# Kernel optimization log

Measured on AMD Instinct MI355X. Metric: run time of the kernel, lower is better.

## Reference

```python
import jax, jax.numpy as jnp
import numpy as np

CHEB_K = 3
DIM_IN = 2
HIDDEN = 64
EMBED_DIM = 10
NODE_NUM = 2048
BATCH = 32


def _gconv(x, supports, W, b, cheb_k=CHEB_K):
    # Chebyshev graph conv applied directly to x (equivalent to building
    # T_k(A) matrices then applying: T_k(A) x = 2 A T_{k-1}(A) x - T_{k-2}(A) x).
    xs = [x, jnp.einsum('nm,bmc->bnc', supports, x)]
    for _ in range(2, cheb_k):
        xs.append(2.0 * jnp.einsum('nm,bmc->bnc', supports, xs[-1]) - xs[-2])
    x_g = jnp.concatenate(xs, axis=-1)          # [B, N, cheb_k*C]
    return jnp.einsum('bni,io->bno', x_g, W) + b


def setup_inputs() -> dict:
    key = jax.random.key(0)
    ks = jax.random.split(key, 7)
    c_in = DIM_IN + HIDDEN                       # 66
    # xavier_normal-ish scale for weights
    def xavier(k, fan_in, fan_out):
        std = float(np.sqrt(2.0 / (fan_in + fan_out)))
        return jax.random.normal(k, (fan_in, fan_out), dtype=jnp.float32) * std
    return {
        'x': jax.random.normal(ks[0], (BATCH, NODE_NUM, DIM_IN), dtype=jnp.float32),
        'state': jax.random.normal(ks[1], (BATCH, NODE_NUM, HIDDEN), dtype=jnp.float32),
        'node_embeddings': jax.random.normal(ks[2], (NODE_NUM, EMBED_DIM), dtype=jnp.float32),
        'W_gate': xavier(ks[3], CHEB_K * c_in, 2 * HIDDEN),
        'b_gate': jnp.zeros((2 * HIDDEN,), dtype=jnp.float32),
        'W_update': xavier(ks[4], CHEB_K * c_in, HIDDEN),
        'b_update': jnp.zeros((HIDDEN,), dtype=jnp.float32),
    }


def reference(x, state, node_embeddings, W_gate, b_gate, W_update, b_update):
    # adaptive adjacency: softmax(relu(E E^T), axis=1)
    logits = jnp.einsum('nc,mc->nm', node_embeddings, node_embeddings)
    supports = jax.nn.softmax(jax.nn.relu(logits), axis=1)   # [N, N]

    input_and_state = jnp.concatenate([x, state], axis=-1)   # [B, N, dim_in+hidden]
    z_r = jax.nn.sigmoid(_gconv(input_and_state, supports, W_gate, b_gate))
    z, r = jnp.split(z_r, 2, axis=-1)                        # each [B, N, hidden]
    candidate = jnp.concatenate([x, z * state], axis=-1)
    hc = jnp.tanh(_gconv(candidate, supports, W_update, b_update))
    h = r * state + (1.0 - r) * hc
    return h
```

## Files before the change

### kernel.cpp

```cpp
#include <hip/hip_runtime.h>


typedef __bf16 bf16x8 __attribute__((ext_vector_type(8)));
typedef __bf16 bf16x4 __attribute__((ext_vector_type(4)));
typedef __bf16 bf16x2 __attribute__((ext_vector_type(2)));
typedef float  f32x4  __attribute__((ext_vector_type(4)));

#define GLB(p) ((__attribute__((address_space(1))) void*)(void*)(p))
#define LDS(p) ((__attribute__((address_space(3))) void*)(p))

__global__ __launch_bounds__(256, 2)
void prologue_kernel(const float* __restrict__ E, __bf16* __restrict__ S,
                     const float* __restrict__ Wg, __bf16* __restrict__ WTg,
                     const float* __restrict__ Wu, __bf16* __restrict__ WTu,
                     const float* __restrict__ x, const float* __restrict__ st,
                     __bf16* __restrict__ T, __bf16* __restrict__ G) {
    const int bid = blockIdx.x;
    const int t = threadIdx.x;
    __shared__ float Ls[66 * 129];
    if (bid >= 2304) {
        const int rb = bid - 2304;
        const int b  = rb >> 4;
        const int n0 = (rb & 15) << 7;
        const size_t mb = (size_t)b * 2048 + n0;
        if (t < 128) {
            const float2 v = *(const float2*)&x[(mb + t) * 2];
            Ls[t] = v.x;
            Ls[129 + t] = v.y;
        }
#pragma unroll
        for (int r = 0; r < 8; ++r) {
            const int task = r * 256 + t;
            const int q = task & 15, n = task >> 4;
            f32x4 v = *(const f32x4*)&st[(mb + n) * 64 + q * 4];
            const int base = (2 + q * 4) * 129 + n;
#pragma unroll
            for (int j = 0; j < 4; ++j) Ls[base + j * 129] = v[j];
        }
        __syncthreads();
#pragma unroll
        for (int r = 0; r < 5; ++r) {
            const int task = r * 256 + t;
            if (task < 1056) {
                const int c = task >> 4, seg = task & 15;
                const float* src = &Ls[c * 129 + seg * 8];
                bf16x8 o;
#pragma unroll
                for (int j = 0; j < 8; ++j) o[j] = (__bf16)src[j];
                *(bf16x8*)&T[(size_t)(b * 66 + c) * 2048 + n0 + seg * 8] = o;
            }
        }
        {
            const int n = t & 127, half = t >> 7;
            const size_t grow = ((size_t)(b * 2048 + n0 + n)) * 256;
            for (int oct = half * 5; oct < (half ? 9 : 5); ++oct) {
                bf16x8 o8;
#pragma unroll
                for (int j = 0; j < 8; ++j) {
                    const int cc = oct * 8 + j;
                    o8[j] = (cc < 66) ? (__bf16)Ls[cc * 129 + n] : (__bf16)0.f;
                }
                *(bf16x8*)&G[grow + oct * 8] = o8;
            }
        }
        return;
    }
    if (bid >= 2048) {
        const float* W = (bid < 2176) ? Wg : Wu;
        __bf16* WT = (bid < 2176) ? WTg : WTu;
        const int Nout = (bid < 2176) ? 128 : 64;
        const int id = (bid - ((bid < 2176) ? 2048 : 2176)) * 256 + t;
        const int o = id >> 8, k = id & 255;
        const int jj = (k >= 144) ? 2 : (k >= 72 ? 1 : 0);
        const int cc = k - 72 * jj;
        const bool ok = (o < Nout) && (cc < 66) && (k < 216);
        float v = 0.f;
        if (ok) {
            if (jj == 0)      v = W[(size_t)cc * Nout + o] - W[(size_t)(132 + cc) * Nout + o];
            else if (jj == 1) v = W[(size_t)(66 + cc) * Nout + o];
            else              v = 2.f * W[(size_t)(132 + cc) * Nout + o];
        }
        WT[id] = (__bf16)v;
        return;
    }
    const int n = bid;
    const int l = t & 63, w = t >> 6;
    float* sm = Ls;
    float* ss = Ls + 4;
    float en[10];
#pragma unroll
    for (int i = 0; i < 10; ++i) en[i] = E[n * 10 + i];
    float vals[8];
    float mx = 0.f;
#pragma unroll
    for (int q = 0; q < 8; ++q) {
        const int m = q * 256 + t;
        const float* em = E + (size_t)m * 10;
        float d = 0.f;
#pragma unroll
        for (int i = 0; i < 10; ++i) d += en[i] * em[i];
        d = fmaxf(d, 0.f);
        vals[q] = d;
        mx = fmaxf(mx, d);
    }
#pragma unroll
    for (int off = 32; off; off >>= 1) mx = fmaxf(mx, __shfl_xor(mx, off));
    if (l == 0) sm[w] = mx;
    __syncthreads();
    mx = fmaxf(fmaxf(sm[0], sm[1]), fmaxf(sm[2], sm[3]));
    float sum = 0.f;
#pragma unroll
    for (int q = 0; q < 8; ++q) { vals[q] = __expf(vals[q] - mx); sum += vals[q]; }
#pragma unroll
    for (int off = 32; off; off >>= 1) sum += __shfl_xor(sum, off);
    if (l == 0) ss[w] = sum;
    __syncthreads();
    sum = ss[0] + ss[1] + ss[2] + ss[3];
    const float inv = 1.f / sum;
#pragma unroll
    for (int q = 0; q < 8; ++q) S[(size_t)n * 2048 + q * 256 + t] = (__bf16)(vals[q] * inv);
}

__global__ __launch_bounds__(256, 3)
void gemm_pipe(const __bf16* __restrict__ A, int lda,
               const __bf16* __restrict__ Bt, int ldb,
               int K, int epi, int swz, int cmode,
               __bf16* __restrict__ outT,
               float* __restrict__ outF, const float* __restrict__ bias,
               const __bf16* __restrict__ zrI,
               const float* __restrict__ state,
               __bf16* __restrict__ Gout, int gsec) {
    __shared__ __align__(16) __bf16 As[2][128 * 64];
    __shared__ __align__(16) __bf16 Bs[2][64 * 64];
    int mt, ct;
    if (swz) { mt = blockIdx.x & 15; ct = blockIdx.x >> 4; }
    else     { mt = blockIdx.x;      ct = blockIdx.y; }
    const int m0 = mt * 128, c0 = ct * 64;
    const int t = threadIdx.x;
    const int l = t & 63, w = t >> 6;
    const int wr = w >> 1, wc = w & 1;
    const int lm = l & 15, kq = l >> 4, lm7 = lm & 7;
    const int sr = l >> 3;
    const int gsw = (l & 7) ^ sr;

    f32x4 acc[4][2];
#pragma unroll
    for (int i = 0; i < 4; ++i)
#pragma unroll
        for (int j = 0; j < 2; ++j) acc[i][j] = (f32x4)0.f;

    const __bf16* Asrc = A  + (size_t)(m0 + w * 8 + sr) * lda + gsw * 8;
    const __bf16* Bsrc = Bt + (size_t)(c0 + w * 8 + sr) * ldb + gsw * 8;
    const int dstA = w * 512 + l * 8;

    auto stage = [&](int buf, int k0) {
#pragma unroll
        for (int q = 0; q < 4; ++q)
            __builtin_amdgcn_global_load_lds(GLB(Asrc + (size_t)q * 32 * lda + k0),
                                             LDS(&As[buf][q * 2048 + dstA]), 16, 0, 0);
#pragma unroll
        for (int q = 0; q < 2; ++q)
            __builtin_amdgcn_global_load_lds(GLB(Bsrc + (size_t)q * 32 * ldb + k0),
                                             LDS(&Bs[buf][q * 2048 + dstA]), 16, 0, 0);
    };
    auto compute = [&](int buf) {
        const __bf16* Ab = &As[buf][0];
        const __bf16* Bb = &Bs[buf][0];
#pragma unroll
        for (int ks = 0; ks < 2; ++ks) {
            const int ga = (((ks << 2) | kq) ^ lm7) << 3;
            bf16x8 af[4], bfr[2];
#pragma unroll
            for (int i = 0; i < 4; ++i)
                af[i] = *(const bf16x8*)&Ab[(wr * 64 + i * 16 + lm) * 64 + ga];
#pragma unroll
            for (int j = 0; j < 2; ++j)
                bfr[j] = *(const bf16x8*)&Bb[(wc * 32 + j * 16 + lm) * 64 + ga];
#pragma unroll
            for (int i = 0; i < 4; ++i)
#pragma unroll
                for (int j = 0; j < 2; ++j)
                    acc[i][j] = __builtin_amdgcn_mfma_f32_16x16x32_bf16(af[i], bfr[j], acc[i][j], 0, 0, 0);
        }
    };

    stage(0, 0);
    const int iters = K >> 6;
    for (int i = 0; i + 2 <= iters; i += 2) {
        stage(1, (i + 1) << 6);
        __builtin_amdgcn_sched_barrier(0);
        __builtin_amdgcn_s_waitcnt(0x0F76);
        __builtin_amdgcn_s_barrier();
        __builtin_amdgcn_sched_barrier(0);
        compute(0);
        __builtin_amdgcn_sched_barrier(0);
        __builtin_amdgcn_s_barrier();
        __builtin_amdgcn_sched_barrier(0);
        if (i + 2 < iters) {
            stage(0, (i + 2) << 6);
            __builtin_amdgcn_sched_barrier(0);
            __builtin_amdgcn_s_waitcnt(0x0F76);
        } else {
            __builtin_amdgcn_s_waitcnt(0x0F70);
        }
        __builtin_amdgcn_s_barrier();
        __builtin_amdgcn_sched_barrier(0);
        compute(1);
        __builtin_amdgcn_sched_barrier(0);
        if (i + 4 <= iters) {
            __builtin_amdgcn_s_barrier();
            __builtin_amdgcn_sched_barrier(0);
        }
    }

    const int rb0 = m0 + wr * 64 + kq * 4;
    const int cb0 = c0 + wc * 32 + lm;
    __bf16* Lt = &As[0][0];
#pragma unroll
    for (int i = 0; i < 4; ++i) {
        const int rbase = rb0 + i * 16;
#pragma unroll
        for (int j = 0; j < 2; ++j) {
            const int c = cb0 + j * 16;
            f32x4 v = acc[i][j];
            if (epi <= 1) {
                bf16x4 pk;
#pragma unroll
                for (int r = 0; r < 4; ++r) pk[r] = (__bf16)v[r];
                if (epi == 0)
                    *(bf16x4*)&outT[(size_t)c * 2048 + rbase] = pk;
                const int mbL = wr * 64 + kq * 4 + i * 16;
                const int clocb = wc * 32 + lm + j * 16;
#pragma unroll
                for (int r = 0; r < 4; ++r) {
                    const int ml = mbL + r;
                    const int swr = (ml & 7) ^ ((ml >> 3) & 7);
                    Lt[ml * 64 + ((((clocb >> 3) ^ swr) & 7) << 3) + (clocb & 7)] = pk[r];
                }
            } else {
                if (c < 64) {
                    const float bb = bias[c];
#pragma unroll
                    for (int r = 0; r < 4; ++r) {
                        const int m = rbase + r;
                        float xx = fminf(fmaxf(v[r] + bb, -15.f), 15.f);
                        float e = __expf(2.f * xx);
                        float hc = (e - 1.f) / (e + 1.f);
                        float rr = (float)zrI[(size_t)m * 64 + c];
                        float s = state[(size_t)m * 64 + c];
                        outF[(size_t)m * 64 + c] = rr * s + (1.f - rr) * hc;
                    }
                }
            }
        }
    }
    if (epi <= 1) {
        __syncthreads();
        const int mloc = t >> 1, h = t & 1;
        const int m = m0 + mloc;
        const int sw = (mloc & 7) ^ ((mloc >> 3) & 7);
#pragma unroll
        for (int k = 0; k < 4; ++k) {
            const int g = h * 4 + k;
            const bf16x8 v = *(const bf16x8*)&Lt[mloc * 64 + ((g ^ sw) & 7) * 8];
            const int c = c0 + g * 8;
            if (cmode) {
                const int b = c >> 6;
                *(bf16x8*)&Gout[((size_t)(b * 2048 + m)) * 256 + gsec + 2 + (c & 63)] = v;
            } else {
                const int b0 = c / 66, b7 = (c + 7) / 66;
                if (b0 == b7) {
                    *(bf16x8*)&Gout[((size_t)(b0 * 2048 + m)) * 256 + gsec + (c - b0 * 66)] = v;
                } else {
#pragma unroll
                    for (int e = 0; e < 8; ++e) {
                        const int ce = c + e, be = ce / 66;
                        Gout[((size_t)(be * 2048 + m)) * 256 + gsec + (ce - be * 66)] = v[e];
                    }
                }
            }
        }
    }
}

__global__ __launch_bounds__(256, 2)
void gemm_w(const __bf16* __restrict__ A,
            const __bf16* __restrict__ Bt,
            __bf16* __restrict__ outT, const float* __restrict__ bias,
            __bf16* __restrict__ zrO,
            const float* __restrict__ state,
            __bf16* __restrict__ Gout,
            const float* __restrict__ xin) {
    __shared__ __align__(16) __bf16 As[2][128 * 64];
    __shared__ __align__(16) __bf16 Bs[2][128 * 64];
    const int m0 = blockIdx.x * 128;
    const int t = threadIdx.x;
    const int l = t & 63, w = t >> 6;
    const int wr = w >> 1, wc = w & 1;
    const int lm = l & 15, kq = l >> 4, lm7 = lm & 7;
    const int sr = l >> 3;
    const int gsw = (l & 7) ^ sr;

    f32x4 acc[4][4];
#pragma unroll
    for (int i = 0; i < 4; ++i)
#pragma unroll
        for (int j = 0; j < 4; ++j) acc[i][j] = (f32x4)0.f;

    const __bf16* Asrc = A  + (size_t)(m0 + w * 8 + sr) * 256 + gsw * 8;
    const __bf16* Bsrc = Bt + (size_t)(w * 8 + sr) * 256 + gsw * 8;
    const int dstA = w * 512 + l * 8;

    auto stage = [&](int buf, int k0) {
#pragma unroll
        for (int q = 0; q < 4; ++q)
            __builtin_amdgcn_global_load_lds(GLB(Asrc + (size_t)q * 32 * 256 + k0),
                                             LDS(&As[buf][q * 2048 + dstA]), 16, 0, 0);
#pragma unroll
        for (int q = 0; q < 4; ++q)
            __builtin_amdgcn_global_load_lds(GLB(Bsrc + (size_t)q * 32 * 256 + k0),
                                             LDS(&Bs[buf][q * 2048 + dstA]), 16, 0, 0);
    };
    auto compute = [&](int buf) {
        const __bf16* Ab = &As[buf][0];
        const __bf16* Bb = &Bs[buf][0];
#pragma unroll
        for (int ks = 0; ks < 2; ++ks) {
            const int ga = (((ks << 2) | kq) ^ lm7) << 3;
            bf16x8 af[4], bfr[4];
#pragma unroll
            for (int i = 0; i < 4; ++i)
                af[i] = *(const bf16x8*)&Ab[(wr * 64 + i * 16 + lm) * 64 + ga];
#pragma unroll
            for (int j = 0; j < 4; ++j)
                bfr[j] = *(const bf16x8*)&Bb[(wc * 64 + j * 16 + lm) * 64 + ga];
#pragma unroll
            for (int i = 0; i < 4; ++i)
#pragma unroll
                for (int j = 0; j < 4; ++j)
                    acc[i][j] = __builtin_amdgcn_mfma_f32_16x16x32_bf16(af[i], bfr[j], acc[i][j], 0, 0, 0);
        }
    };

    stage(0, 0);
    const int iters = 4;
    for (int i = 0; i + 2 <= iters; i += 2) {
        stage(1, (i + 1) << 6);
        __builtin_amdgcn_sched_barrier(0);
        __builtin_amdgcn_s_waitcnt(0x0F78);
        __builtin_amdgcn_s_barrier();
        __builtin_amdgcn_sched_barrier(0);
        compute(0);
        __builtin_amdgcn_sched_barrier(0);
        __builtin_amdgcn_s_barrier();
        __builtin_amdgcn_sched_barrier(0);
        if (i + 2 < iters) {
            stage(0, (i + 2) << 6);
            __builtin_amdgcn_sched_barrier(0);
            __builtin_amdgcn_s_waitcnt(0x0F78);
        } else {
            __builtin_amdgcn_s_waitcnt(0x0F70);
        }
        __builtin_amdgcn_s_barrier();
        __builtin_amdgcn_sched_barrier(0);
        compute(1);
        __builtin_amdgcn_sched_barrier(0);
        if (i + 4 <= iters) {
            __builtin_amdgcn_s_barrier();
            __builtin_amdgcn_sched_barrier(0);
        }
    }

    const int rb0 = m0 + wr * 64 + kq * 4;
    const int cb0 = wc * 64 + lm;
    __bf16* Lt = &As[0][0];
#pragma unroll
    for (int i = 0; i < 4; ++i) {
        const int rbase = rb0 + i * 16;
#pragma unroll
        for (int j = 0; j < 4; ++j) {
            const int c = cb0 + j * 16;
            f32x4 v = acc[i][j];
            const float bb = bias[c];
            if (c < 64) {
                const int b = rbase >> 11, n = rbase & 2047;
                bf16x4 pk;
#pragma unroll
                for (int r = 0; r < 4; ++r) {
                    float xx = fminf(fmaxf(v[r] + bb, -30.f), 30.f);
                    const float z = 1.f / (1.f + __expf(-xx));
                    const float sv = state[(size_t)(rbase + r) * 64 + c];
                    pk[r] = (__bf16)(z * sv);
                }
                *(bf16x4*)&outT[(size_t)(b * 64 + c) * 2048 + n] = pk;
                const int mbL = wr * 64 + kq * 4 + i * 16;
#pragma unroll
                for (int r = 0; r < 4; ++r) {
                    const int ml = mbL + r;
                    const int swr = (ml & 7) ^ ((ml >> 3) & 7);
                    Lt[ml * 64 + ((((c >> 3) ^ swr) & 7) << 3) + (c & 7)] = pk[r];
                }
            } else {
#pragma unroll
                for (int r = 0; r < 4; ++r) {
                    float xx = fminf(fmaxf(v[r] + bb, -30.f), 30.f);
                    zrO[(size_t)(rbase + r) * 64 + (c - 64)] = (__bf16)(1.f / (1.f + __expf(-xx)));
                }
            }
        }
    }
    __syncthreads();
    {
        const int mloc = t >> 1, h = t & 1;
        const int m = m0 + mloc;
        const int sw = (mloc & 7) ^ ((mloc >> 3) & 7);
        const size_t gr = (size_t)m * 256;
        auto ldg = [&](int g) { return *(const bf16x8*)&Lt[mloc * 64 + ((g ^ sw) & 7) * 8]; };
        if (h == 0) {
            const float2 vx = *(const float2*)&xin[(size_t)m * 2];
            const bf16x8 g0 = ldg(0), g1 = ldg(1), g2 = ldg(2), g3 = ldg(3), g4 = ldg(4);
            bf16x8 o;
            o[0] = (__bf16)vx.x; o[1] = (__bf16)vx.y;
#pragma unroll
            for (int e = 0; e < 6; ++e) o[2 + e] = g0[e];
            *(bf16x8*)&Gout[gr + 0] = o;
            o[0] = g0[6]; o[1] = g0[7];
#pragma unroll
            for (int e = 0; e < 6; ++e) o[2 + e] = g1[e];
            *(bf16x8*)&Gout[gr + 8] = o;
            o[0] = g1[6]; o[1] = g1[7];
#pragma unroll
            for (int e = 0; e < 6; ++e) o[2 + e] = g2[e];
            *(bf16x8*)&Gout[gr + 16] = o;
            o[0] = g2[6]; o[1] = g2[7];
#pragma unroll
            for (int e = 0; e < 6; ++e) o[2 + e] = g3[e];
            *(bf16x8*)&Gout[gr + 24] = o;
            o[0] = g3[6]; o[1] = g3[7];
#pragma unroll
            for (int e = 0; e < 6; ++e) o[2 + e] = g4[e];
            *(bf16x8*)&Gout[gr + 32] = o;
        } else {
            const bf16x8 v4 = ldg(4), v5 = ldg(5), v6 = ldg(6), v7 = ldg(7);
            bf16x8 o;
            o[0] = v4[6]; o[1] = v4[7];
#pragma unroll
            for (int e = 0; e < 6; ++e) o[2 + e] = v5[e];
            *(bf16x8*)&Gout[gr + 40] = o;
            o[0] = v5[6]; o[1] = v5[7];
#pragma unroll
            for (int e = 0; e < 6; ++e) o[2 + e] = v6[e];
            *(bf16x8*)&Gout[gr + 48] = o;
            o[0] = v6[6]; o[1] = v6[7];
#pragma unroll
            for (int e = 0; e < 6; ++e) o[2 + e] = v7[e];
            *(bf16x8*)&Gout[gr + 56] = o;
            o[0] = v7[6]; o[1] = v7[7];
#pragma unroll
            for (int e = 0; e < 6; ++e) o[2 + e] = (__bf16)0.f;
            *(bf16x8*)&Gout[gr + 64] = o;
            *(bf16x2*)&Gout[gr + 72]  = *(const bf16x2*)&A[gr + 72];
            *(bf16x2*)&Gout[gr + 144] = *(const bf16x2*)&A[gr + 144];
        }
    }
}

extern "C" void kernel_launch(void* const* d_in, const int* in_sizes, int n_in,
                              void* d_out, int out_size, void* d_ws, size_t ws_size,
                              hipStream_t stream) {
    (void)in_sizes; (void)n_in; (void)out_size; (void)ws_size;
    const float* x  = (const float*)d_in[0];
    const float* st = (const float*)d_in[1];
    const float* E  = (const float*)d_in[2];
    const float* Wg = (const float*)d_in[3];
    const float* bg = (const float*)d_in[4];
    const float* Wu = (const float*)d_in[5];
    const float* bu = (const float*)d_in[6];
    float* out = (float*)d_out;

    char* p = (char*)d_ws;
    __bf16* S   = (__bf16*)p; p += (size_t)2048 * 2048 * 2;
    __bf16* T0  = (__bf16*)p; p += (size_t)2112 * 2048 * 2;
    __bf16* T1  = (__bf16*)p; p += (size_t)2112 * 2048 * 2;
    __bf16* Gg  = (__bf16*)p; p += (size_t)65536 * 256 * 2;
    __bf16* Gu  = (__bf16*)p; p += (size_t)65536 * 256 * 2;
    __bf16* ZR  = (__bf16*)p; p += (size_t)65536 * 64 * 2;
    __bf16* WTg = (__bf16*)p; p += 128 * 256 * 2;
    __bf16* WTu = (__bf16*)p; p += 128 * 256 * 2;

    prologue_kernel<<<2816, 256, 0, stream>>>(E, S, Wg, WTg, Wu, WTu, x, st, T0, Gg);

    gemm_pipe<<<528, 256, 0, stream>>>(S, 2048, T0, 2048, 2048, 0, 1, 0, T1, nullptr, nullptr, nullptr, nullptr, Gg, 72);
    gemm_pipe<<<528, 256, 0, stream>>>(S, 2048, T1, 2048, 2048, 1, 1, 0, nullptr, nullptr, nullptr, nullptr, nullptr, Gg, 144);
    gemm_w<<<512, 256, 0, stream>>>(Gg, WTg, T0, bg, ZR, st, Gu, x);

    gemm_pipe<<<512, 256, 0, stream>>>(S, 2048, T0, 2048, 2048, 0, 1, 1, T1, nullptr, nullptr, nullptr, nullptr, Gu, 72);
    gemm_pipe<<<512, 256, 0, stream>>>(S, 2048, T1, 2048, 2048, 1, 1, 1, nullptr, nullptr, nullptr, nullptr, nullptr, Gu, 144);
    gemm_pipe<<<dim3(512, 1), 256, 0, stream>>>(Gu, 256, WTu, 256, 256, 3, 0, 0, nullptr, out, bu, ZR, st, nullptr, 0);
}
```

Before: 261.5 us.

## Prefetch state tile into LDS during gemm_w tail; write Gout directly from registers

In gemm_w, the state tile for the block is loaded asynchronously into the now-free LDS A/B stage-0 buffers during the last compute iteration, and the epilogue reads state from LDS instead of doing scattered global loads. The transpose staging buffer moves to As[1]. In the other GEMM epilogue, the LDS-transposed, vectorized Gout write is replaced by direct scalar bf16 stores from accumulator registers, removing a __syncthreads and an LDS round trip. That trade gives up coalescing on the Gout stores.

```diff
diff --git a/kernel.cpp b/kernel.cpp
--- a/kernel.cpp
+++ b/kernel.cpp
@@ -215,7 +215,6 @@
 
     const int rb0 = m0 + wr * 64 + kq * 4;
     const int cb0 = c0 + wc * 32 + lm;
-    __bf16* Lt = &As[0][0];
 #pragma unroll
     for (int i = 0; i < 4; ++i) {
         const int rbase = rb0 + i * 16;
@@ -229,14 +228,12 @@
                 for (int r = 0; r < 4; ++r) pk[r] = (__bf16)v[r];
                 if (epi == 0)
                     *(bf16x4*)&outT[(size_t)c * 2048 + rbase] = pk;
-                const int mbL = wr * 64 + kq * 4 + i * 16;
-                const int clocb = wc * 32 + lm + j * 16;
-#pragma unroll
-                for (int r = 0; r < 4; ++r) {
-                    const int ml = mbL + r;
-                    const int swr = (ml & 7) ^ ((ml >> 3) & 7);
-                    Lt[ml * 64 + ((((clocb >> 3) ^ swr) & 7) << 3) + (clocb & 7)] = pk[r];
-                }
+                int b, gcol;
+                if (cmode) { b = c >> 6;  gcol = gsec + 2 + (c & 63); }
+                else       { b = c / 66;  gcol = gsec + (c - b * 66); }
+                const size_t gb = ((size_t)(b * 2048 + rbase)) * 256 + gcol;
+#pragma unroll
+                for (int r = 0; r < 4; ++r) Gout[gb + (size_t)r * 256] = pk[r];
             } else {
                 if (c < 64) {
                     const float bb = bias[c];
@@ -249,33 +246,6 @@
                         float rr = (float)zrI[(size_t)m * 64 + c];
                         float s = state[(size_t)m * 64 + c];
                         outF[(size_t)m * 64 + c] = rr * s + (1.f - rr) * hc;
-                    }
-                }
-            }
-        }
-    }
-    if (epi <= 1) {
-        __syncthreads();
-        const int mloc = t >> 1, h = t & 1;
-        const int m = m0 + mloc;
-        const int sw = (mloc & 7) ^ ((mloc >> 3) & 7);
-#pragma unroll
-        for (int k = 0; k < 4; ++k) {
-            const int g = h * 4 + k;
-            const bf16x8 v = *(const bf16x8*)&Lt[mloc * 64 + ((g ^ sw) & 7) * 8];
-            const int c = c0 + g * 8;
-            if (cmode) {
-                const int b = c >> 6;
-                *(bf16x8*)&Gout[((size_t)(b * 2048 + m)) * 256 + gsec + 2 + (c & 63)] = v;
-            } else {
-                const int b0 = c / 66, b7 = (c + 7) / 66;
-                if (b0 == b7) {
-                    *(bf16x8*)&Gout[((size_t)(b0 * 2048 + m)) * 256 + gsec + (c - b0 * 66)] = v;
-                } else {
-#pragma unroll
-                    for (int e = 0; e < 8; ++e) {
-                        const int ce = c + e, be = ce / 66;
-                        Gout[((size_t)(be * 2048 + m)) * 256 + gsec + (ce - be * 66)] = v[e];
                     }
                 }
             }
@@ -321,6 +291,17 @@
             __builtin_amdgcn_global_load_lds(GLB(Bsrc + (size_t)q * 32 * 256 + k0),
                                              LDS(&Bs[buf][q * 2048 + dstA]), 16, 0, 0);
     };
+    auto stage_state = [&]() {
+        const float* Ssrc = state + (size_t)m0 * 64 + t * 4;
+#pragma unroll
+        for (int q = 0; q < 4; ++q)
+            __builtin_amdgcn_global_load_lds(GLB(Ssrc + q * 1024),
+                                             LDS((char*)&As[0][0] + t * 16 + q * 4096), 16, 0, 0);
+#pragma unroll
+        for (int q = 0; q < 4; ++q)
+            __builtin_amdgcn_global_load_lds(GLB(Ssrc + (q + 4) * 1024),
+                                             LDS((char*)&Bs[0][0] + t * 16 + q * 4096), 16, 0, 0);
+    };
     auto compute = [&](int buf) {
         const __bf16* Ab = &As[buf][0];
         const __bf16* Bb = &Bs[buf][0];
@@ -363,6 +344,10 @@
         }
         __builtin_amdgcn_s_barrier();
         __builtin_amdgcn_sched_barrier(0);
+        if (i + 2 >= iters) {
+            stage_state();
+            __builtin_amdgcn_sched_barrier(0);
+        }
         compute(1);
         __builtin_amdgcn_sched_barrier(0);
         if (i + 4 <= iters) {
@@ -370,10 +355,14 @@
             __builtin_amdgcn_sched_barrier(0);
         }
     }
+    __builtin_amdgcn_s_waitcnt(0x0F70);
+    __builtin_amdgcn_s_barrier();
+    __builtin_amdgcn_sched_barrier(0);
 
     const int rb0 = m0 + wr * 64 + kq * 4;
     const int cb0 = wc * 64 + lm;
-    __bf16* Lt = &As[0][0];
+    __bf16* Lt = &As[1][0];
+    const float* Sld = wr ? (const float*)&Bs[0][0] : (const float*)&As[0][0];
 #pragma unroll
     for (int i = 0; i < 4; ++i) {
         const int rbase = rb0 + i * 16;
@@ -389,7 +378,7 @@
                 for (int r = 0; r < 4; ++r) {
                     float xx = fminf(fmaxf(v[r] + bb, -30.f), 30.f);
                     const float z = 1.f / (1.f + __expf(-xx));
-                    const float sv = state[(size_t)(rbase + r) * 64 + c];
+                    const float sv = Sld[(kq * 4 + i * 16 + r) * 64 + c];
                     pk[r] = (__bf16)(z * sv);
                 }
                 *(bf16x4*)&outT[(size_t)(b * 64 + c) * 2048 + n] = pk;
```

After: 253.2 us. -3.2%, faster.
